# Kernel tuning notes

Measured on AMD Instinct MI355X. Metric: run time of the kernel, lower is better.

## Reference

```python
import jax, jax.numpy as jnp
import numpy as np

N, E, H, IN, ED = 10000, 160000, 8, 128, 32
C1, C2 = 128, 128  # per-head channels of conv1 and conv2_1


def gat_conv(x, edge_index, edge_attr, W, We, att_s, att_d, att_e, bias, concat):
    """PyG GATConv with edge_dim, add_self_loops=True (fill_value='mean'), eval mode."""
    n = x.shape[0]
    h, c = att_s.shape
    src, dst = edge_index[0], edge_index[1]
    # self-loop edge_attr = per-node mean of incoming edge attrs (PyG fill_value='mean')
    deg = jax.ops.segment_sum(jnp.ones((src.shape[0],), x.dtype), dst, num_segments=n)
    loop_attr = jax.ops.segment_sum(edge_attr, dst, num_segments=n) / jnp.maximum(deg, 1.0)[:, None]
    loop = jnp.arange(n)
    src = jnp.concatenate([src, loop])
    dst = jnp.concatenate([dst, loop])
    ea = jnp.concatenate([edge_attr, loop_attr], axis=0)  # [E+N, ED]

    xh = (x @ W).reshape(n, h, c)                  # [N,H,C]
    a_s = jnp.sum(xh * att_s, axis=-1)             # [N,H]
    a_d = jnp.sum(xh * att_d, axis=-1)             # [N,H]
    eh = (ea @ We).reshape(-1, h, c)               # [E+N,H,C]
    a_e = jnp.sum(eh * att_e, axis=-1)             # [E+N,H]

    alpha = jax.nn.leaky_relu(a_s[src] + a_d[dst] + a_e, negative_slope=0.2)
    # segment softmax over incoming edges of each dst node (every node has a self loop)
    amax = jax.ops.segment_max(alpha, dst, num_segments=n)
    ex = jnp.exp(alpha - amax[dst])
    denom = jax.ops.segment_sum(ex, dst, num_segments=n)
    alpha = ex / (denom[dst] + 1e-16)

    out = jax.ops.segment_sum(xh[src] * alpha[:, :, None], dst, num_segments=n)  # [N,H,C]
    out = out.reshape(n, h * c) if concat else out.mean(axis=1)
    return out + bias


def setup_inputs() -> dict:
    key = jax.random.key(0)
    ks = jax.random.split(key, 16)
    s = 0.05
    return {
        "x": jax.random.normal(ks[0], (N, IN), jnp.float32),
        "edge_index": jax.random.randint(ks[1], (2, E), 0, N, dtype=jnp.int64),
        "edge_attr": jax.random.normal(ks[2], (E, ED), jnp.float32),
        # conv1: IN -> H*C1, concat=True
        "W1": jax.random.normal(ks[3], (IN, H * C1), jnp.float32) * s,
        "We1": jax.random.normal(ks[4], (ED, H * C1), jnp.float32) * s,
        "as1": jax.random.normal(ks[5], (H, C1), jnp.float32) * s,
        "ad1": jax.random.normal(ks[6], (H, C1), jnp.float32) * s,
        "ae1": jax.random.normal(ks[7], (H, C1), jnp.float32) * s,
        "b1": jnp.zeros((H * C1,), jnp.float32),
        # conv2_1: H*C1 -> C2, concat=False (Drugbank branch)
        "W2": jax.random.normal(ks[8], (H * C1, H * C2), jnp.float32) * s,
        "We2": jax.random.normal(ks[9], (ED, H * C2), jnp.float32) * s,
        "as2": jax.random.normal(ks[10], (H, C2), jnp.float32) * s,
        "ad2": jax.random.normal(ks[11], (H, C2), jnp.float32) * s,
        "ae2": jax.random.normal(ks[12], (H, C2), jnp.float32) * s,
        "b2": jnp.zeros((C2,), jnp.float32),
    }


def reference(x, edge_index, edge_attr, W1, We1, as1, ad1, ae1, b1,
              W2, We2, as2, ad2, ae2, b2):
    # dataset == 'Drugbank' path; dropout is identity in eval mode
    h = gat_conv(x, edge_index, edge_attr, W1, We1, as1, ad1, ae1, b1, concat=True)
    h = jax.nn.relu(h)
    out = gat_conv(h, edge_index, edge_attr, W2, We2, as2, ad2, ae2, b2, concat=False)
    return out
```

## Files before the change

kernel.cpp:

```cpp
#include <hip/hip_runtime.h>
#include <hip/hip_bf16.h>
#include <cstdint>
#include <cstddef>


#define EDD 32

typedef __attribute__((ext_vector_type(4))) float f32x4;
typedef __attribute__((ext_vector_type(8))) short bf16x8;
typedef __attribute__((ext_vector_type(8))) unsigned short u16x8;

__device__ inline unsigned short f2bf_rn(float f) {
  uint32_t u = __float_as_uint(f);
  return (unsigned short)((u + 0x7FFFu + ((u >> 16) & 1u)) >> 16);
}

__device__ inline float bf2f(unsigned short b) {
  return __uint_as_float(((uint32_t)b) << 16);
}

__device__ inline void gload_lds16(const void* g, void* l) {
  __builtin_amdgcn_global_load_lds((const __attribute__((address_space(1))) void*)g,
                                   (__attribute__((address_space(3))) void*)l, 16, 0, 0);
}


__global__ void deg_count_kernel(const int* __restrict__ ei, int* __restrict__ deg, int E) {
  int e = blockIdx.x * 256 + threadIdx.x;
  if (e < E) atomicAdd(&deg[ei[E + e]], 1);
}

__global__ void scan_kernel(const int* __restrict__ deg, int* __restrict__ rowptr,
                            int* __restrict__ cursor, int n) {
  __shared__ int wsum[16];
  int t = threadIdx.x;
  int chunk = (n + 1023) >> 10;
  int lo = min(t * chunk, n), hi = min(lo + chunk, n);
  int s = 0;
  for (int i = lo; i < hi; ++i) s += deg[i];
  int lane = t & 63, w = t >> 6;
  int v = s;
#pragma unroll
  for (int off = 1; off < 64; off <<= 1) {
    int u = __shfl_up(v, off);
    if (lane >= off) v += u;
  }
  if (lane == 63) wsum[w] = v;
  __syncthreads();
  if (t == 0) {
    int acc = 0;
#pragma unroll
    for (int i = 0; i < 16; ++i) { int x = wsum[i]; wsum[i] = acc; acc += x; }
  }
  __syncthreads();
  int excl = v - s + wsum[w];
  for (int i = lo; i < hi; ++i) {
    rowptr[i] = excl; cursor[i] = excl; excl += deg[i];
  }
  if (t == 1023) rowptr[n] = excl;
}

__global__ void scatter_kernel(const int* __restrict__ ei, int* __restrict__ cursor,
                               int* __restrict__ csr_src, int* __restrict__ csr_eid, int E) {
  int e = blockIdx.x * 256 + threadIdx.x;
  if (e >= E) return;
  int d = ei[E + e];
  int pos = atomicAdd(&cursor[d], 1);
  csr_src[pos] = ei[e];
  csr_eid[pos] = e;
}

__global__ void permute_ea_kernel(const int* __restrict__ csr_eid,
                                  const float* __restrict__ edge_attr,
                                  float* __restrict__ ea_csr, int E) {
  int gid = blockIdx.x * 256 + threadIdx.x;
  if (gid >= E * 8) return;
  int p = gid >> 3, q = gid & 7;
  int e = csr_eid[p];
  ((float4*)ea_csr)[(size_t)p * 8 + q] = ((const float4*)edge_attr)[(size_t)e * 8 + q];
}


__global__ void cvt_bf16_kernel(const float* __restrict__ in,
                                unsigned short* __restrict__ out, int n4) {
  int i = blockIdx.x * 256 + threadIdx.x;
  if (i >= n4) return;
  float4 v = ((const float4*)in)[i];
  ushort4 o;
  o.x = f2bf_rn(v.x); o.y = f2bf_rn(v.y); o.z = f2bf_rn(v.z); o.w = f2bf_rn(v.w);
  ((ushort4*)out)[i] = o;
}

__global__ void transpose_both_kernel(const float* __restrict__ W1, unsigned short* __restrict__ Bt1,
                                      const float* __restrict__ W2, unsigned short* __restrict__ Bt2) {
  __shared__ float tile[32][33];
  int by = blockIdx.y;
  const float* W; unsigned short* Bt; int K, bk;
  if (by < 4) { W = W1; Bt = Bt1; K = 128; bk = by * 32; }
  else        { W = W2; Bt = Bt2; K = 1024; bk = (by - 4) * 32; }
  int bn = blockIdx.x * 32;
  int tx = threadIdx.x & 31, ty = threadIdx.x >> 5;
  for (int r = ty; r < 32; r += 8)
    tile[r][tx] = W[(size_t)(bk + r) * 1024 + bn + tx];
  __syncthreads();
  for (int r = ty; r < 32; r += 8)
    Bt[(size_t)(bn + r) * K + bk + tx] = f2bf_rn(tile[tx][r]);
}

__global__ void ve_both_kernel(const float* __restrict__ We1, const float* __restrict__ ae1,
                               const float* __restrict__ We2, const float* __restrict__ ae2,
                               float* __restrict__ Ve) {
  int b = blockIdx.x;
  const float* We = b ? We2 : We1;
  const float* ae = b ? ae2 : ae1;
  int t = threadIdx.x;
  int d = t >> 3, h = t & 7;
  float s = 0.f;
  for (int c = 0; c < 128; ++c) s = fmaf(We[d * 1024 + h * 128 + c], ae[h * 128 + c], s);
  Ve[b * 256 + t] = s;
}


__global__ __launch_bounds__(256) void gemm1_fullk_kernel(
    const unsigned short* __restrict__ Abf, const unsigned short* __restrict__ Btbf,
    unsigned short* __restrict__ Cbf, float* __restrict__ a_s, float* __restrict__ a_d,
    const float* __restrict__ att_s, const float* __restrict__ att_d, int M) {
  __shared__ __align__(16) unsigned short lds[4 * 8192];
  __shared__ float redS[128][2];
  __shared__ float redD[128][2];
  const int t = threadIdx.x;
  const int lane = t & 63;
  const int wid = t >> 6;
  const int wr = wid >> 1, wc = wid & 1;
  const int m0 = blockIdx.y * 128;
  const int n0 = blockIdx.x * 128;
  const int hb = blockIdx.x;
  const int srow = lane >> 2;
  const int sg = lane & 3;

#pragma unroll
  for (int s = 0; s < 4; ++s) {
    unsigned short* L = lds + s * 8192;
    int k0 = s * 32;
#pragma unroll
    for (int q = 0; q < 2; ++q) {
      int rb = wid * 32 + q * 16;
      int row = rb + srow;
      int gsrc = sg ^ ((row >> 1) & 3);
      size_t ga = (size_t)(m0 + row) * 128 + k0 + gsrc * 8;
      size_t gb = (size_t)(n0 + row) * 128 + k0 + gsrc * 8;
      gload_lds16(Abf + ga, L + rb * 32);
      gload_lds16(Btbf + gb, L + 4096 + rb * 32);
    }
  }
  __syncthreads();

  int offa[4], offb[4];
#pragma unroll
  for (int i = 0; i < 4; ++i) {
    int rowa = wr * 64 + i * 16 + (lane & 15);
    offa[i] = rowa * 32 + (((lane >> 4) ^ ((rowa >> 1) & 3)) * 8);
    int rowb = wc * 64 + i * 16 + (lane & 15);
    offb[i] = rowb * 32 + (((lane >> 4) ^ ((rowb >> 1) & 3)) * 8);
  }

  f32x4 acc[4][4] = {};
#pragma unroll
  for (int s = 0; s < 4; ++s) {
    unsigned short* L = lds + s * 8192;
    bf16x8 ah[4];
#pragma unroll
    for (int i = 0; i < 4; ++i) ah[i] = *(const bf16x8*)(L + offa[i]);
#pragma unroll
    for (int j = 0; j < 4; ++j) {
      bf16x8 bh = *(const bf16x8*)(L + 4096 + offb[j]);
#pragma unroll
      for (int i = 0; i < 4; ++i)
        acc[i][j] = __builtin_amdgcn_mfma_f32_16x16x32_bf16(ah[i], bh, acc[i][j], 0, 0, 0);
    }
  }

  float as_v[4], ad_v[4];
#pragma unroll
  for (int j = 0; j < 4; ++j) {
    int c = n0 + wc * 64 + j * 16 + (lane & 15);
    as_v[j] = att_s[c];
    ad_v[j] = att_d[c];
  }
#pragma unroll
  for (int i = 0; i < 4; ++i) {
#pragma unroll
    for (int r = 0; r < 4; ++r) {
      float sA = 0.f, sD = 0.f;
#pragma unroll
      for (int j = 0; j < 4; ++j) {
        sA = fmaf(acc[i][j][r], as_v[j], sA);
        sD = fmaf(acc[i][j][r], ad_v[j], sD);
      }
#pragma unroll
      for (int mask = 1; mask <= 8; mask <<= 1) {
        sA += __shfl_xor(sA, mask);
        sD += __shfl_xor(sD, mask);
      }
      if ((lane & 15) == 0) {
        int ml = wr * 64 + i * 16 + (lane >> 4) * 4 + r;
        redS[ml][wc] = sA;
        redD[ml][wc] = sD;
      }
      int m = m0 + wr * 64 + i * 16 + (lane >> 4) * 4 + r;
      if (m < M) {
#pragma unroll
        for (int j = 0; j < 4; ++j) {
          int n = n0 + wc * 64 + j * 16 + (lane & 15);
          Cbf[(size_t)m * 1024 + n] = f2bf_rn(acc[i][j][r]);
        }
      }
    }
  }
  __syncthreads();
  if (t < 128) {
    int m = m0 + t;
    if (m < M) {
      a_s[(size_t)m * 8 + hb] = redS[t][0] + redS[t][1];
      a_d[(size_t)m * 8 + hb] = redD[t][0] + redD[t][1];
    }
  }
}


__global__ __launch_bounds__(256) void gemm2_dbuf_kernel(
    const unsigned short* __restrict__ Abf, const unsigned short* __restrict__ Btbf,
    unsigned short* __restrict__ Cbf, float* __restrict__ a_s, float* __restrict__ a_d,
    const float* __restrict__ att_s, const float* __restrict__ att_d, int M, int K) {
  __shared__ __align__(16) unsigned short lds[2 * 8192];
  __shared__ float redS[128][2];
  __shared__ float redD[128][2];
  const int t = threadIdx.x;
  const int lane = t & 63;
  const int wid = t >> 6;
  const int wr = wid >> 1, wc = wid & 1;
  const int m0 = blockIdx.y * 128;
  const int n0 = blockIdx.x * 128;
  const int hb = blockIdx.x;
  const int srow = lane >> 2;
  const int sg = lane & 3;
  const int nk = K >> 5;

  auto stage = [&](int b, int k) {
    unsigned short* L = lds + b * 8192;
    int k0 = k * 32;
#pragma unroll
    for (int q = 0; q < 2; ++q) {
      int rb = wid * 32 + q * 16;
      int row = rb + srow;
      int gsrc = sg ^ ((row >> 1) & 3);
      size_t ga = (size_t)(m0 + row) * K + k0 + gsrc * 8;
      size_t gb = (size_t)(n0 + row) * K + k0 + gsrc * 8;
      gload_lds16(Abf + ga, L + rb * 32);
      gload_lds16(Btbf + gb, L + 4096 + rb * 32);
    }
  };

  int offa[4], offb[4];
#pragma unroll
  for (int i = 0; i < 4; ++i) {
    int rowa = wr * 64 + i * 16 + (lane & 15);
    offa[i] = rowa * 32 + (((lane >> 4) ^ ((rowa >> 1) & 3)) * 8);
    int rowb = wc * 64 + i * 16 + (lane & 15);
    offb[i] = rowb * 32 + (((lane >> 4) ^ ((rowb >> 1) & 3)) * 8);
  }

  f32x4 acc[4][4] = {};
  stage(0, 0);
  __syncthreads();

  for (int k = 0; k < nk; ++k) {
    if (k + 1 < nk) stage((k + 1) & 1, k + 1);
    unsigned short* L = lds + (k & 1) * 8192;
    bf16x8 ah[4], bh[4];
#pragma unroll
    for (int i = 0; i < 4; ++i) ah[i] = *(const bf16x8*)(L + offa[i]);
#pragma unroll
    for (int j = 0; j < 4; ++j) bh[j] = *(const bf16x8*)(L + 4096 + offb[j]);
#pragma unroll
    for (int j = 0; j < 4; ++j)
#pragma unroll
      for (int i = 0; i < 4; ++i)
        acc[i][j] = __builtin_amdgcn_mfma_f32_16x16x32_bf16(ah[i], bh[j], acc[i][j], 0, 0, 0);
    __syncthreads();
  }

  float as_v[4], ad_v[4];
#pragma unroll
  for (int j = 0; j < 4; ++j) {
    int c = n0 + wc * 64 + j * 16 + (lane & 15);
    as_v[j] = att_s[c];
    ad_v[j] = att_d[c];
  }
#pragma unroll
  for (int i = 0; i < 4; ++i) {
#pragma unroll
    for (int r = 0; r < 4; ++r) {
      float sA = 0.f, sD = 0.f;
#pragma unroll
      for (int j = 0; j < 4; ++j) {
        sA = fmaf(acc[i][j][r], as_v[j], sA);
        sD = fmaf(acc[i][j][r], ad_v[j], sD);
      }
#pragma unroll
      for (int mask = 1; mask <= 8; mask <<= 1) {
        sA += __shfl_xor(sA, mask);
        sD += __shfl_xor(sD, mask);
      }
      if ((lane & 15) == 0) {
        int ml = wr * 64 + i * 16 + (lane >> 4) * 4 + r;
        redS[ml][wc] = sA;
        redD[ml][wc] = sD;
      }
      int m = m0 + wr * 64 + i * 16 + (lane >> 4) * 4 + r;
      if (m < M) {
#pragma unroll
        for (int j = 0; j < 4; ++j) {
          int n = n0 + wc * 64 + j * 16 + (lane & 15);
          Cbf[(size_t)m * 1024 + n] = f2bf_rn(acc[i][j][r]);
        }
      }
    }
  }
  __syncthreads();
  if (t < 128) {
    int m = m0 + t;
    if (m < M) {
      a_s[(size_t)m * 8 + hb] = redS[t][0] + redS[t][1];
      a_d[(size_t)m * 8 + hb] = redD[t][0] + redD[t][1];
    }
  }
}


__global__ __launch_bounds__(256) void alpha_sm_kernel(
    const int* __restrict__ rowptr, const int* __restrict__ csr_src,
    const float* __restrict__ ea_csr,
    const float* __restrict__ a_s, const float* __restrict__ a_d,
    const float* __restrict__ Ve,
    float* __restrict__ alpha_t, float* __restrict__ self_t, int N, int E) {
  __shared__ float sVe[EDD][8];
  int t = threadIdx.x;
  sVe[t >> 3][t & 7] = Ve[t];
  __syncthreads();
  int n = blockIdx.x * 4 + (t >> 6);
  if (n >= N) return;
  int lane = t & 63;
  int e8 = lane >> 3, h = lane & 7;
  int r0 = rowptr[n], deg = rowptr[n + 1] - r0;
  float adn = a_d[(size_t)n * 8 + h];
  float m = -1e30f, s = 0.f, aesum = 0.f;
  for (int i = e8; i < deg; i += 8) {
    int p = r0 + i;
    int src = csr_src[p];
    const float4* ea4 = (const float4*)(ea_csr + (size_t)p * EDD);
    float ae = 0.f;
#pragma unroll
    for (int k = 0; k < 8; ++k) {
      float4 v = ea4[k];
      ae = fmaf(v.x, sVe[k * 4 + 0][h], ae);
      ae = fmaf(v.y, sVe[k * 4 + 1][h], ae);
      ae = fmaf(v.z, sVe[k * 4 + 2][h], ae);
      ae = fmaf(v.w, sVe[k * 4 + 3][h], ae);
    }
    aesum += ae;
    float a = a_s[(size_t)src * 8 + h] + adn + ae;
    a = (a > 0.f) ? a : 0.2f * a;
    alpha_t[(size_t)h * E + p] = a;
    if (a <= m) {
      s += __expf(a - m);
    } else {
      s = s * __expf(m - a) + 1.f;
      m = a;
    }
  }
#pragma unroll
  for (int mask = 8; mask <= 32; mask <<= 1) {
    float mo = __shfl_xor(m, mask);
    float so = __shfl_xor(s, mask);
    aesum += __shfl_xor(aesum, mask);
    float mn = fmaxf(m, mo);
    s = s * __expf(m - mn) + so * __expf(mo - mn);
    m = mn;
  }
  float aeself = aesum / fmaxf((float)deg, 1.f);
  float aself = a_s[(size_t)n * 8 + h] + adn + aeself;
  aself = (aself > 0.f) ? aself : 0.2f * aself;
  float mn = fmaxf(m, aself);
  s = s * __expf(m - mn) + __expf(aself - mn);
  float inv = 1.f / (s + 1e-16f);
  if (e8 == 0) self_t[(size_t)h * N + n] = __expf(aself - mn) * inv;
  for (int i = e8; i < deg; i += 8) {
    size_t p = (size_t)h * E + r0 + i;
    alpha_t[p] = __expf(alpha_t[p] - mn) * inv;
  }
}


template <int RELU_BIAS>
__global__ __launch_bounds__(256) void agg_gather_h_kernel(
    const unsigned short* __restrict__ xbf, const float* __restrict__ alpha_t,
    const float* __restrict__ self_t, const int* __restrict__ rowptr,
    const int* __restrict__ csr_src, const float* __restrict__ bias,
    unsigned short* __restrict__ obf, int N, int E) {
  __shared__ int ls_idx[512];
  __shared__ float ls_w[512];
  const int h = blockIdx.x & 7;
  const int g = blockIdx.x >> 3;
  const int t = threadIdx.x;
  const int nb = g * 16;
  const int n = nb + (t >> 4);
  const int sub = t & 15;
  const bool live = (n < N);
  const int r_start = rowptr[nb];
  const int r_end = rowptr[min(nb + 16, N)];
  int r0 = 0, r1 = 0;
  if (live) { r0 = rowptr[n]; r1 = rowptr[n + 1]; }
  const float* __restrict__ pw = alpha_t + (size_t)h * E;
  const size_t cb = (size_t)h * 128 + sub * 8;
  float acc[8] = {0.f, 0.f, 0.f, 0.f, 0.f, 0.f, 0.f, 0.f};
  if (live) {
    float ws = self_t[(size_t)h * N + n];
    u16x8 v = *(const u16x8*)(xbf + (size_t)n * 1024 + cb);
#pragma unroll
    for (int k = 0; k < 8; ++k) acc[k] = ws * bf2f(v[k]);
  }
  for (int base = r_start; base < r_end; base += 512) {
    int cnt = min(512, r_end - base);
    for (int i = t; i < cnt; i += 256) {
      ls_idx[i] = csr_src[base + i];
      ls_w[i] = pw[base + i];
    }
    __syncthreads();
    if (live) {
      int lo = max(r0, base), hi = min(r1, base + cnt);
      int p = lo;
      for (; p + 4 <= hi; p += 4) {
        int q0 = p - base;
        float w0 = ls_w[q0], w1 = ls_w[q0 + 1], w2 = ls_w[q0 + 2], w3 = ls_w[q0 + 3];
        int s0 = ls_idx[q0], s1 = ls_idx[q0 + 1], s2 = ls_idx[q0 + 2], s3 = ls_idx[q0 + 3];
        u16x8 v0 = *(const u16x8*)(xbf + (size_t)s0 * 1024 + cb);
        u16x8 v1 = *(const u16x8*)(xbf + (size_t)s1 * 1024 + cb);
        u16x8 v2 = *(const u16x8*)(xbf + (size_t)s2 * 1024 + cb);
        u16x8 v3 = *(const u16x8*)(xbf + (size_t)s3 * 1024 + cb);
#pragma unroll
        for (int k = 0; k < 8; ++k) acc[k] = fmaf(w0, bf2f(v0[k]), acc[k]);
#pragma unroll
        for (int k = 0; k < 8; ++k) acc[k] = fmaf(w1, bf2f(v1[k]), acc[k]);
#pragma unroll
        for (int k = 0; k < 8; ++k) acc[k] = fmaf(w2, bf2f(v2[k]), acc[k]);
#pragma unroll
        for (int k = 0; k < 8; ++k) acc[k] = fmaf(w3, bf2f(v3[k]), acc[k]);
      }
      for (; p < hi; ++p) {
        int q0 = p - base;
        float w0 = ls_w[q0];
        int s0 = ls_idx[q0];
        u16x8 v0 = *(const u16x8*)(xbf + (size_t)s0 * 1024 + cb);
#pragma unroll
        for (int k = 0; k < 8; ++k) acc[k] = fmaf(w0, bf2f(v0[k]), acc[k]);
      }
    }
    __syncthreads();
  }
  if (!live) return;
  u16x8 o;
  if (RELU_BIAS) {
    float4 b0 = *(const float4*)(bias + cb);
    float4 b1v = *(const float4*)(bias + cb + 4);
    float bb[8] = {b0.x, b0.y, b0.z, b0.w, b1v.x, b1v.y, b1v.z, b1v.w};
#pragma unroll
    for (int k = 0; k < 8; ++k) o[k] = f2bf_rn(fmaxf(acc[k] + bb[k], 0.f));
  } else {
#pragma unroll
    for (int k = 0; k < 8; ++k) o[k] = f2bf_rn(acc[k]);
  }
  *(u16x8*)(obf + (size_t)n * 1024 + cb) = o;
}


__global__ void head_reduce_kernel(const unsigned short* __restrict__ xpart,
                                   const float* __restrict__ b2,
                                   float* __restrict__ outp, int N) {
  int gid = blockIdx.x * 256 + threadIdx.x;
  if (gid >= N * 32) return;
  int n = gid >> 5, q = gid & 31;
  float sx = 0.f, sy = 0.f, sz = 0.f, sw = 0.f;
#pragma unroll
  for (int h = 0; h < 8; ++h) {
    ushort4 v = *(const ushort4*)(xpart + (size_t)n * 1024 + h * 128 + q * 4);
    sx += bf2f(v.x); sy += bf2f(v.y); sz += bf2f(v.z); sw += bf2f(v.w);
  }
  float4 b = ((const float4*)b2)[q];
  float4 o;
  o.x = sx * 0.125f + b.x;
  o.y = sy * 0.125f + b.y;
  o.z = sz * 0.125f + b.z;
  o.w = sw * 0.125f + b.w;
  ((float4*)outp)[(size_t)n * 32 + q] = o;
}


extern "C" void kernel_launch(void* const* d_in, const int* in_sizes, int n_in,
                              void* d_out, int out_size, void* d_ws, size_t ws_size,
                              hipStream_t stream) {
  const float* x        = (const float*)d_in[0];
  const int*   ei       = (const int*)d_in[1];
  const float* edge_attr= (const float*)d_in[2];
  const float* W1       = (const float*)d_in[3];
  const float* We1      = (const float*)d_in[4];
  const float* as1      = (const float*)d_in[5];
  const float* ad1      = (const float*)d_in[6];
  const float* ae1      = (const float*)d_in[7];
  const float* b1       = (const float*)d_in[8];
  const float* W2       = (const float*)d_in[9];
  const float* We2      = (const float*)d_in[10];
  const float* as2      = (const float*)d_in[11];
  const float* ad2      = (const float*)d_in[12];
  const float* ae2      = (const float*)d_in[13];
  const float* b2       = (const float*)d_in[14];
  float* out = (float*)d_out;

  const int N = in_sizes[0] / 128;
  const int E = in_sizes[2] / EDD;
  const int Mpad = ((N + 127) / 128) * 128;

  char* ws = (char*)d_ws;
  size_t off = 0;
  auto alloc = [&](size_t bytes) -> void* {
    void* p = ws + off;
    off = (off + bytes + 255) & ~(size_t)255;
    return p;
  };
  int*   deg       = (int*)alloc((size_t)N * 4);
  int*   rowptr    = (int*)alloc((size_t)(N + 1) * 4);
  int*   cursor    = (int*)alloc((size_t)N * 4);
  int*   csr_src   = (int*)alloc((size_t)E * 4);
  int*   csr_eid   = (int*)alloc((size_t)E * 4);
  float* ea_csr    = (float*)alloc((size_t)E * EDD * 4);
  float* a_s       = (float*)alloc((size_t)N * 8 * 4);
  float* a_d       = (float*)alloc((size_t)N * 8 * 4);
  float* Ve        = (float*)alloc(512 * 4);
  float* alpha_t   = (float*)alloc((size_t)E * 8 * 4);
  float* self_t    = (float*)alloc((size_t)N * 8 * 4);
  unsigned short* xh1bf = (unsigned short*)alloc((size_t)N * 1024 * 2);
  unsigned short* xh2bf = (unsigned short*)alloc((size_t)N * 1024 * 2);
  unsigned short* xpart = (unsigned short*)alloc((size_t)N * 1024 * 2);
  unsigned short* xbf   = (unsigned short*)alloc((size_t)Mpad * 128 * 2);
  unsigned short* Bt1   = (unsigned short*)alloc((size_t)1024 * 128 * 2);
  unsigned short* Bt2   = (unsigned short*)alloc((size_t)1024 * 1024 * 2);
  unsigned short* h1bf  = (unsigned short*)alloc((size_t)Mpad * 1024 * 2);
  (void)ws_size; (void)n_in; (void)out_size;

  hipMemsetAsync(deg, 0, (size_t)N * 4, stream);

  int gE = (E + 255) / 256;
  deg_count_kernel<<<gE, 256, 0, stream>>>(ei, deg, E);
  scan_kernel<<<1, 1024, 0, stream>>>(deg, rowptr, cursor, N);
  scatter_kernel<<<gE, 256, 0, stream>>>(ei, cursor, csr_src, csr_eid, E);
  permute_ea_kernel<<<(E * 8 + 255) / 256, 256, 0, stream>>>(csr_eid, edge_attr, ea_csr, E);

  cvt_bf16_kernel<<<(N * 128 / 4 + 255) / 256, 256, 0, stream>>>(x, xbf, N * 128 / 4);
  transpose_both_kernel<<<dim3(32, 36), 256, 0, stream>>>(W1, Bt1, W2, Bt2);
  ve_both_kernel<<<2, 256, 0, stream>>>(We1, ae1, We2, ae2, Ve);

  dim3 ggrid(8, Mpad / 128);
  int gSM = (N + 3) / 4;
  int gAG = 8 * ((N + 15) / 16);

  gemm1_fullk_kernel<<<ggrid, 256, 0, stream>>>(xbf, Bt1, xh1bf, a_s, a_d, as1, ad1, N);
  alpha_sm_kernel<<<gSM, 256, 0, stream>>>(rowptr, csr_src, ea_csr, a_s, a_d, Ve,
                                           alpha_t, self_t, N, E);
  agg_gather_h_kernel<1><<<gAG, 256, 0, stream>>>(xh1bf, alpha_t, self_t, rowptr, csr_src,
                                                  b1, h1bf, N, E);

  gemm2_dbuf_kernel<<<ggrid, 256, 0, stream>>>(h1bf, Bt2, xh2bf, a_s, a_d, as2, ad2, N, 1024);
  alpha_sm_kernel<<<gSM, 256, 0, stream>>>(rowptr, csr_src, ea_csr, a_s, a_d, Ve + 256,
                                           alpha_t, self_t, N, E);
  agg_gather_h_kernel<0><<<gAG, 256, 0, stream>>>(xh2bf, alpha_t, self_t, rowptr, csr_src,
                                                  nullptr, xpart, N, E);
  head_reduce_kernel<<<(N * 32 + 255) / 256, 256, 0, stream>>>(xpart, b2, out, N);
}
```

Baseline: 211.0 us.

## Split K across two warp groups in gemm2 with LDS partial-sum reduction

```diff
diff --git a/kernel.cpp b/kernel.cpp
--- a/kernel.cpp
+++ b/kernel.cpp
@@ -228,30 +228,33 @@
 }
 
 
-__global__ __launch_bounds__(256) void gemm2_dbuf_kernel(
+__global__ __launch_bounds__(512) void gemm2_dbuf_kernel(
     const unsigned short* __restrict__ Abf, const unsigned short* __restrict__ Btbf,
     unsigned short* __restrict__ Cbf, float* __restrict__ a_s, float* __restrict__ a_d,
     const float* __restrict__ att_s, const float* __restrict__ att_d, int M, int K) {
-  __shared__ __align__(16) unsigned short lds[2 * 8192];
+  __shared__ __align__(16) unsigned short lds[2 * 16384];
   __shared__ float redS[128][2];
   __shared__ float redD[128][2];
   const int t = threadIdx.x;
   const int lane = t & 63;
   const int wid = t >> 6;
-  const int wr = wid >> 1, wc = wid & 1;
+  const int kb = wid >> 2;
+  const int wq = wid & 3;
+  const int wr = wq >> 1, wc = wq & 1;
   const int m0 = blockIdx.y * 128;
   const int n0 = blockIdx.x * 128;
   const int hb = blockIdx.x;
   const int srow = lane >> 2;
   const int sg = lane & 3;
-  const int nk = K >> 5;
+  const int kbase = kb * (K >> 1);
+  const int nk = K >> 6;
 
   auto stage = [&](int b, int k) {
-    unsigned short* L = lds + b * 8192;
-    int k0 = k * 32;
+    unsigned short* L = lds + kb * 16384 + b * 8192;
+    int k0 = kbase + k * 32;
 #pragma unroll
     for (int q = 0; q < 2; ++q) {
-      int rb = wid * 32 + q * 16;
+      int rb = wq * 32 + q * 16;
       int row = rb + srow;
       int gsrc = sg ^ ((row >> 1) & 3);
       size_t ga = (size_t)(m0 + row) * K + k0 + gsrc * 8;
@@ -276,7 +279,7 @@
 
   for (int k = 0; k < nk; ++k) {
     if (k + 1 < nk) stage((k + 1) & 1, k + 1);
-    unsigned short* L = lds + (k & 1) * 8192;
+    unsigned short* L = lds + kb * 16384 + (k & 1) * 8192;
     bf16x8 ah[4], bh[4];
 #pragma unroll
     for (int i = 0; i < 4; ++i) ah[i] = *(const bf16x8*)(L + offa[i]);
@@ -290,39 +293,60 @@
     __syncthreads();
   }
 
-  float as_v[4], ad_v[4];
-#pragma unroll
-  for (int j = 0; j < 4; ++j) {
-    int c = n0 + wc * 64 + j * 16 + (lane & 15);
-    as_v[j] = att_s[c];
-    ad_v[j] = att_d[c];
-  }
-#pragma unroll
-  for (int i = 0; i < 4; ++i) {
-#pragma unroll
-    for (int r = 0; r < 4; ++r) {
-      float sA = 0.f, sD = 0.f;
+  float* cmb = (float*)lds;
+  if (kb == 0) {
+    float* dst = cmb + wq * 4096 + lane * 64;
+#pragma unroll
+    for (int i = 0; i < 4; ++i)
+#pragma unroll
+      for (int j = 0; j < 4; ++j)
+        *(f32x4*)(dst + (i * 4 + j) * 4) = acc[i][j];
+  }
+  __syncthreads();
+  if (kb == 1) {
+    const float* src = cmb + wq * 4096 + lane * 64;
+#pragma unroll
+    for (int i = 0; i < 4; ++i)
 #pragma unroll
       for (int j = 0; j < 4; ++j) {
-        sA = fmaf(acc[i][j][r], as_v[j], sA);
-        sD = fmaf(acc[i][j][r], ad_v[j], sD);
-      }
-#pragma unroll
-      for (int mask = 1; mask <= 8; mask <<= 1) {
-        sA += __shfl_xor(sA, mask);
-        sD += __shfl_xor(sD, mask);
-      }
-      if ((lane & 15) == 0) {
-        int ml = wr * 64 + i * 16 + (lane >> 4) * 4 + r;
-        redS[ml][wc] = sA;
-        redD[ml][wc] = sD;
-      }
-      int m = m0 + wr * 64 + i * 16 + (lane >> 4) * 4 + r;
-      if (m < M) {
+        f32x4 p = *(const f32x4*)(src + (i * 4 + j) * 4);
+        acc[i][j] += p;
+      }
+
+    float as_v[4], ad_v[4];
+#pragma unroll
+    for (int j = 0; j < 4; ++j) {
+      int c = n0 + wc * 64 + j * 16 + (lane & 15);
+      as_v[j] = att_s[c];
+      ad_v[j] = att_d[c];
+    }
+#pragma unroll
+    for (int i = 0; i < 4; ++i) {
+#pragma unroll
+      for (int r = 0; r < 4; ++r) {
+        float sA = 0.f, sD = 0.f;
 #pragma unroll
         for (int j = 0; j < 4; ++j) {
-          int n = n0 + wc * 64 + j * 16 + (lane & 15);
-          Cbf[(size_t)m * 1024 + n] = f2bf_rn(acc[i][j][r]);
+          sA = fmaf(acc[i][j][r], as_v[j], sA);
+          sD = fmaf(acc[i][j][r], ad_v[j], sD);
+        }
+#pragma unroll
+        for (int mask = 1; mask <= 8; mask <<= 1) {
+          sA += __shfl_xor(sA, mask);
+          sD += __shfl_xor(sD, mask);
+        }
+        if ((lane & 15) == 0) {
+          int ml = wr * 64 + i * 16 + (lane >> 4) * 4 + r;
+          redS[ml][wc] = sA;
+          redD[ml][wc] = sD;
+        }
+        int m = m0 + wr * 64 + i * 16 + (lane >> 4) * 4 + r;
+        if (m < M) {
+#pragma unroll
+          for (int j = 0; j < 4; ++j) {
+            int n = n0 + wc * 64 + j * 16 + (lane & 15);
+            Cbf[(size_t)m * 1024 + n] = f2bf_rn(acc[i][j][r]);
+          }
         }
       }
     }
@@ -579,7 +603,7 @@
   agg_gather_h_kernel<1><<<gAG, 256, 0, stream>>>(xh1bf, alpha_t, self_t, rowptr, csr_src,
                                                   b1, h1bf, N, E);
 
-  gemm2_dbuf_kernel<<<ggrid, 256, 0, stream>>>(h1bf, Bt2, xh2bf, a_s, a_d, as2, ad2, N, 1024);
+  gemm2_dbuf_kernel<<<ggrid, 512, 0, stream>>>(h1bf, Bt2, xh2bf, a_s, a_d, as2, ad2, N, 1024);
   alpha_sm_kernel<<<gSM, 256, 0, stream>>>(rowptr, csr_src, ea_csr, a_s, a_d, Ve + 256,
                                            alpha_t, self_t, N, E);
   agg_gather_h_kernel<0><<<gAG, 256, 0, stream>>>(xh2bf, alpha_t, self_t, rowptr, csr_src,
```

Measured after the change: 240.8 us. 1.14x slower.
